# Optimization experiments

Hardware: AMD Instinct MI355X
Metric: run time of the kernel (lower is better)

Reference implementation:

```python
import jax, jax.numpy as jnp
import numpy as np

FANOUT = 10
NT = [61952, 5632, 512]      # targets produced by layer i
NN = [681472, 61952, 5632]   # input nodes consumed by layer i
NE = [619520, 56320, 5120]   # sampled edges for layer i (NT[i]*FANOUT)
IN_DIM = 256
HID = 256
NCLS = 47
EPS = 1e-5


def setup_inputs() -> dict:
    key = jax.random.key(0)
    ks = jax.random.split(key, 16)
    inp = {}
    inp['x_feat'] = jax.random.normal(ks[0], (NN[0], IN_DIM), jnp.float32)
    for i in range(3):
        # each target samples exactly FANOUT neighbors -> dst is repeat(arange)
        inp[f'src{i}'] = jax.random.randint(ks[1 + i], (NE[i],), 0, NN[i], dtype=jnp.int32)
        inp[f'dst{i}'] = jnp.repeat(jnp.arange(NT[i], dtype=jnp.int32), FANOUT)
        inp[f'tlid{i}'] = jax.random.randint(ks[4 + i], (NT[i],), 0, NN[i], dtype=jnp.int32)
        d_in = IN_DIM if i == 0 else HID
        s = 1.0 / np.sqrt(d_in)
        inp[f'Wl{i}'] = jax.random.uniform(ks[7 + i], (d_in, HID), jnp.float32, -s, s)
        inp[f'Wr{i}'] = jax.random.uniform(ks[10 + i], (d_in, HID), jnp.float32, -s, s)
        inp[f'b{i}'] = jnp.zeros((HID,), jnp.float32)
        inp[f'g{i}'] = jnp.ones((HID,), jnp.float32)
        inp[f'be{i}'] = jnp.zeros((HID,), jnp.float32)
    sf = 1.0 / np.sqrt(HID)
    inp['fc_w'] = jax.random.uniform(ks[13], (HID, NCLS), jnp.float32, -sf, sf)
    inp['fc_b'] = jnp.zeros((NCLS,), jnp.float32)
    return inp


def _sage_bn_relu(x, src, dst, tlid, Wl, Wr, b, g, be, n_t):
    # gather neighbor messages and mean-aggregate per target (SAGEConv, mean aggr)
    msg = x[src]                                               # [E, d_in]
    agg = jax.ops.segment_sum(msg, dst, num_segments=n_t)      # [T, d_in]
    cnt = jax.ops.segment_sum(jnp.ones(src.shape, x.dtype), dst, num_segments=n_t)
    agg = agg / jnp.maximum(cnt, 1.0)[:, None]
    x_tgt = x[tlid]                                            # F.embedding gather of target feats
    h = agg @ Wl + x_tgt @ Wr + b                              # lin_l(agg) + lin_r(x_target)
    # BatchNorm1d in training mode (biased batch stats)
    mu = h.mean(axis=0)
    var = h.var(axis=0)
    h = (h - mu) * jax.lax.rsqrt(var + EPS) * g + be
    return jax.nn.relu(h)


def reference(x_feat, src0, dst0, tlid0, src1, dst1, tlid1, src2, dst2, tlid2,
              Wl0, Wr0, b0, g0, be0, Wl1, Wr1, b1, g1, be1, Wl2, Wr2, b2, g2, be2,
              fc_w, fc_b):
    x = x_feat
    layers = [
        (src0, dst0, tlid0, Wl0, Wr0, b0, g0, be0, NT[0]),
        (src1, dst1, tlid1, Wl1, Wr1, b1, g1, be1, NT[1]),
        (src2, dst2, tlid2, Wl2, Wr2, b2, g2, be2, NT[2]),
    ]
    for (src, dst, tlid, Wl, Wr, b, g, be, n_t) in layers:
        x = _sage_bn_relu(x, src, dst, tlid, Wl, Wr, b, g, be, n_t)
    out = x @ fc_w + fc_b                                      # [B, class_count]
    return out
```

## Files before the change

### kernel.cpp

```cpp
#include <hip/hip_runtime.h>

#define HID 256
#define FANOUT 10

typedef __attribute__((ext_vector_type(8))) short bf16x8;
typedef __attribute__((ext_vector_type(4))) float f32x4;

__device__ __forceinline__ unsigned short f2bf(float f) {
    unsigned int u = __float_as_uint(f);
    u += 0x7FFFu + ((u >> 16) & 1u);
    return (unsigned short)(u >> 16);
}

__device__ __forceinline__ void gld_lds16(const void* g, void* l) {
    __builtin_amdgcn_global_load_lds((const __attribute__((address_space(1))) void*)g,
                                     (__attribute__((address_space(3))) void*)l, 16, 0, 0);
}

__global__ __launch_bounds__(256)
void agg_gather_kernel(const float* __restrict__ x, const int* __restrict__ src,
                       const int* __restrict__ tlid, unsigned short* __restrict__ Ag,
                       int T, const float* __restrict__ scal,
                       const float* __restrict__ shft, int apply) {
    const int wave = threadIdx.x >> 6, lane = threadIdx.x & 63;
    const int t = blockIdx.x * 4 + wave;
    if (t >= T) return;
    const float4* x4 = (const float4*)x;
    float4 sc = make_float4(1.f, 1.f, 1.f, 1.f);
    float4 sh = make_float4(0.f, 0.f, 0.f, 0.f);
    if (apply) {
        sc = ((const float4*)scal)[lane];
        sh = ((const float4*)shft)[lane];
    }
    const int* sp = src + (size_t)t * FANOUT;
    float sx = 0.f, sy = 0.f, sz = 0.f, sw = 0.f;
#pragma unroll
    for (int j = 0; j < FANOUT; ++j) {
        float4 v = x4[(size_t)sp[j] * 64 + lane];
        if (apply) {
            v.x = fmaxf(fmaf(v.x, sc.x, sh.x), 0.f);
            v.y = fmaxf(fmaf(v.y, sc.y, sh.y), 0.f);
            v.z = fmaxf(fmaf(v.z, sc.z, sh.z), 0.f);
            v.w = fmaxf(fmaf(v.w, sc.w, sh.w), 0.f);
        }
        sx += v.x; sy += v.y; sz += v.z; sw += v.w;
    }
    float4 tv = x4[(size_t)tlid[t] * 64 + lane];
    if (apply) {
        tv.x = fmaxf(fmaf(tv.x, sc.x, sh.x), 0.f);
        tv.y = fmaxf(fmaf(tv.y, sc.y, sh.y), 0.f);
        tv.z = fmaxf(fmaf(tv.z, sc.z, sh.z), 0.f);
        tv.w = fmaxf(fmaf(tv.w, sc.w, sh.w), 0.f);
    }

    const int rb = t >> 6;
    const int i  = (t & 63) >> 4;
    const int m0 = t & 15;
    const int cl   = lane >> 3;
    const int quad = (lane >> 1) & 3;
    const int j0   = (lane & 1) * 4;
    const int lf   = quad * 16 + m0;
    const size_t base = (size_t)rb * 32768 + (size_t)i * 512 + (size_t)lf * 8 + j0;

    ushort4 oa, ot;
    oa.x = f2bf(sx * 0.1f); oa.y = f2bf(sy * 0.1f);
    oa.z = f2bf(sz * 0.1f); oa.w = f2bf(sw * 0.1f);
    ot.x = f2bf(tv.x); ot.y = f2bf(tv.y); ot.z = f2bf(tv.z); ot.w = f2bf(tv.w);
    *(ushort4*)&Ag[base + (size_t)cl * 2048]       = oa;
    *(ushort4*)&Ag[base + (size_t)(cl + 8) * 2048] = ot;
}

__global__ __launch_bounds__(256)
void convw_all_kernel(const float* __restrict__ Wl0, const float* __restrict__ Wr0,
                      const float* __restrict__ Wl1, const float* __restrict__ Wr1,
                      const float* __restrict__ Wl2, const float* __restrict__ Wr2,
                      unsigned short* __restrict__ Wt) {
    const int idx = blockIdx.x * 256 + threadIdx.x;
    const int layer = idx >> 17, r = idx & 131071;
    const float* Wl = (layer == 0) ? Wl0 : (layer == 1) ? Wl1 : Wl2;
    const float* Wr = (layer == 0) ? Wr0 : (layer == 1) ? Wr1 : Wr2;
    const int kc = r & 31, n = (r >> 5) & 255, c = r >> 13;
    const int k = c * 32 + kc;
    const float v = (k < 256) ? Wl[k * 256 + n] : Wr[(k - 256) * 256 + n];
    Wt[idx] = f2bf(v);
}

__global__ __launch_bounds__(256)
void gemm_mfma_kernel(const unsigned short* __restrict__ Ag,
                      const unsigned short* __restrict__ Wt,
                      float* __restrict__ hbuf,
                      float* __restrict__ ssum, float* __restrict__ ssq) {
    __shared__ unsigned short Alds[2048];
    __shared__ unsigned short Blds[8192];
    const int tid = threadIdx.x, wave = tid >> 6, lane = tid & 63;
    const size_t rb = blockIdx.x;

    f32x4 acc[4][4];
#pragma unroll
    for (int a = 0; a < 4; ++a)
#pragma unroll
        for (int b = 0; b < 4; ++b) acc[a][b] = (f32x4){0.f, 0.f, 0.f, 0.f};

    const unsigned short* Abase = Ag + rb * 32768;
    const int soff = wave * 512 + lane * 8;

    for (int c = 0; c < 16; ++c) {
        __syncthreads();
        gld_lds16(Abase + (size_t)c * 2048 + soff, &Alds[wave * 512]);
        const unsigned short* Bb = Wt + (size_t)c * 8192;
#pragma unroll
        for (int ii = 0; ii < 4; ++ii)
            gld_lds16(Bb + ii * 2048 + soff, &Blds[ii * 2048 + wave * 512]);
        __syncthreads();

        bf16x8 af[4], bfr[4];
#pragma unroll
        for (int mi = 0; mi < 4; ++mi)
            af[mi] = *(const bf16x8*)&Alds[(mi * 64 + lane) * 8];
        const int nb = wave * 64 + (lane & 15);
        const int ko = (lane >> 4) * 8;
#pragma unroll
        for (int t = 0; t < 4; ++t)
            bfr[t] = *(const bf16x8*)&Blds[(nb + t * 16) * 32 + ko];

#pragma unroll
        for (int mi = 0; mi < 4; ++mi)
#pragma unroll
            for (int t = 0; t < 4; ++t)
                acc[mi][t] = __builtin_amdgcn_mfma_f32_16x16x32_bf16(
                    af[mi], bfr[t], acc[mi][t], 0, 0, 0);
    }

    const int q = lane >> 4, m0 = lane & 15;

#pragma unroll
    for (int t = 0; t < 4; ++t) {
        const int col = wave * 64 + t * 16 + m0;
#pragma unroll
        for (int mi = 0; mi < 4; ++mi) {
            float* op = hbuf + (rb * 64 + (size_t)mi * 16 + q * 4) * 256 + col;
#pragma unroll
            for (int r = 0; r < 4; ++r)
                op[(size_t)r * 256] = acc[mi][t][r];
        }
    }

    float s[4], sq[4];
#pragma unroll
    for (int t = 0; t < 4; ++t) {
        float a = 0.f, b = 0.f;
#pragma unroll
        for (int mi = 0; mi < 4; ++mi)
#pragma unroll
            for (int r = 0; r < 4; ++r) {
                const float v = acc[mi][t][r];
                a += v; b += v * v;
            }
        s[t] = a; sq[t] = b;
    }
#pragma unroll
    for (int t = 0; t < 4; ++t) {
        s[t] += __shfl_xor(s[t], 16);  s[t] += __shfl_xor(s[t], 32);
        sq[t] += __shfl_xor(sq[t], 16); sq[t] += __shfl_xor(sq[t], 32);
    }
    if (lane < 16) {
#pragma unroll
        for (int t = 0; t < 4; ++t) {
            const int col = wave * 64 + t * 16 + m0;
            atomicAdd(&ssum[col], s[t]);
            atomicAdd(&ssq[col], sq[t]);
        }
    }
}

__global__ void zero_kernel(float* p) { p[threadIdx.x] = 0.f; }

__global__ void bnfin_kernel(const float* __restrict__ ssum, const float* __restrict__ ssq,
                             const float* __restrict__ g, const float* __restrict__ be,
                             float* __restrict__ scal, float* __restrict__ shft,
                             float invT) {
    const int c = threadIdx.x;
    const float mu = ssum[c] * invT;
    float var = ssq[c] * invT - mu * mu;
    var = fmaxf(var, 0.f);
    const float rs = rsqrtf(var + 1e-5f);
    const float sc = rs * g[c];
    scal[c] = sc;
    shft[c] = be[c] - mu * sc;
}

__global__ __launch_bounds__(64)
void fc_kernel(const float* __restrict__ x, const float* __restrict__ scal,
               const float* __restrict__ shft, const float* __restrict__ w,
               const float* __restrict__ b, float* __restrict__ out, int C) {
    __shared__ float row[HID];
    const int r = blockIdx.x;
    const int tid = threadIdx.x;
    float4 v = ((const float4*)(x + (size_t)r * HID))[tid];
    const float4 sc = ((const float4*)scal)[tid];
    const float4 sh = ((const float4*)shft)[tid];
    v.x = fmaxf(fmaf(v.x, sc.x, sh.x), 0.f);
    v.y = fmaxf(fmaf(v.y, sc.y, sh.y), 0.f);
    v.z = fmaxf(fmaf(v.z, sc.z, sh.z), 0.f);
    v.w = fmaxf(fmaf(v.w, sc.w, sh.w), 0.f);
    ((float4*)row)[tid] = v;
    __syncthreads();
    if (tid < C) {
        float acc = b[tid];
#pragma unroll 8
        for (int k = 0; k < HID; ++k)
            acc = fmaf(row[k], w[k * C + tid], acc);
        out[(size_t)r * C + tid] = acc;
    }
}

extern "C" void kernel_launch(void* const* d_in, const int* in_sizes, int n_in,
                              void* d_out, int out_size, void* d_ws, size_t ws_size,
                              hipStream_t stream) {
    const float* x_feat = (const float*)d_in[0];
    const int T0 = in_sizes[3];
    const int T1 = in_sizes[11];
    const int T2 = in_sizes[19];
    const int NCLS = in_sizes[26];

    float* buf0 = (float*)d_ws;
    float* buf1 = buf0 + (size_t)T0 * HID;
    float* buf2 = buf1 + (size_t)T1 * HID;
    float* ssum = buf2 + (size_t)T2 * HID;
    float* ssq  = ssum + HID;
    float* scal = ssq + HID;
    float* shft = scal + HID;
    unsigned short* Wt = (unsigned short*)(shft + HID + 256);
    unsigned short* Ag = Wt + 3 * 512 * 256;

    const float* xs[3]   = { x_feat, buf0, buf1 };
    float*       bufs[3] = { buf0, buf1, buf2 };
    const int    Ts[3]   = { T0, T1, T2 };

    convw_all_kernel<<<1536, 256, 0, stream>>>(
        (const float*)d_in[4],  (const float*)d_in[5],
        (const float*)d_in[12], (const float*)d_in[13],
        (const float*)d_in[20], (const float*)d_in[21], Wt);

    for (int i = 0; i < 3; ++i) {
        const int base = 1 + i * 8;
        const int*   src  = (const int*)d_in[base + 0];
        const int*   tlid = (const int*)d_in[base + 2];
        const float* g    = (const float*)d_in[base + 6];
        const float* be   = (const float*)d_in[base + 7];
        const int T = Ts[i];

        agg_gather_kernel<<<(T + 3) / 4, 256, 0, stream>>>(
            xs[i], src, tlid, Ag, T, scal, shft, i > 0 ? 1 : 0);
        zero_kernel<<<1, 512, 0, stream>>>(ssum);
        gemm_mfma_kernel<<<T / 64, 256, 0, stream>>>(
            Ag, Wt + (size_t)i * 131072, bufs[i], ssum, ssq);
        bnfin_kernel<<<1, HID, 0, stream>>>(ssum, ssq, g, be, scal, shft, 1.0f / (float)T);
    }

    const float* fc_w = (const float*)d_in[25];
    const float* fc_b = (const float*)d_in[26];
    fc_kernel<<<T2, 64, 0, stream>>>(buf2, scal, shft, fc_w, fc_b, (float*)d_out, NCLS);
}
```

Baseline: 1.063 ms.

## Fuse neighbor gather-aggregation into GEMM kernel via shared-memory A tile

Merges the gather/mean-aggregate kernel into the MFMA GEMM kernel. Each block builds its full 64x512 bf16 A tile in LDS (64 KB) from the gathered features, then runs the GEMM reading B fragments directly from global memory instead of staging them through LDS. This removes the global write and read of the intermediate Ag buffer and one launch per layer. In exchange, each wave gathers its 16 targets serially, so there is less memory-level parallelism per block, and the large LDS footprint lowers occupancy.

After: 1.027 ms. 1.04x faster.

```diff
diff --git a/kernel.cpp b/kernel.cpp
--- a/kernel.cpp
+++ b/kernel.cpp
@@ -10,64 +10,6 @@
     unsigned int u = __float_as_uint(f);
     u += 0x7FFFu + ((u >> 16) & 1u);
     return (unsigned short)(u >> 16);
-}
-
-__device__ __forceinline__ void gld_lds16(const void* g, void* l) {
-    __builtin_amdgcn_global_load_lds((const __attribute__((address_space(1))) void*)g,
-                                     (__attribute__((address_space(3))) void*)l, 16, 0, 0);
-}
-
-__global__ __launch_bounds__(256)
-void agg_gather_kernel(const float* __restrict__ x, const int* __restrict__ src,
-                       const int* __restrict__ tlid, unsigned short* __restrict__ Ag,
-                       int T, const float* __restrict__ scal,
-                       const float* __restrict__ shft, int apply) {
-    const int wave = threadIdx.x >> 6, lane = threadIdx.x & 63;
-    const int t = blockIdx.x * 4 + wave;
-    if (t >= T) return;
-    const float4* x4 = (const float4*)x;
-    float4 sc = make_float4(1.f, 1.f, 1.f, 1.f);
-    float4 sh = make_float4(0.f, 0.f, 0.f, 0.f);
-    if (apply) {
-        sc = ((const float4*)scal)[lane];
-        sh = ((const float4*)shft)[lane];
-    }
-    const int* sp = src + (size_t)t * FANOUT;
-    float sx = 0.f, sy = 0.f, sz = 0.f, sw = 0.f;
-#pragma unroll
-    for (int j = 0; j < FANOUT; ++j) {
-        float4 v = x4[(size_t)sp[j] * 64 + lane];
-        if (apply) {
-            v.x = fmaxf(fmaf(v.x, sc.x, sh.x), 0.f);
-            v.y = fmaxf(fmaf(v.y, sc.y, sh.y), 0.f);
-            v.z = fmaxf(fmaf(v.z, sc.z, sh.z), 0.f);
-            v.w = fmaxf(fmaf(v.w, sc.w, sh.w), 0.f);
-        }
-        sx += v.x; sy += v.y; sz += v.z; sw += v.w;
-    }
-    float4 tv = x4[(size_t)tlid[t] * 64 + lane];
-    if (apply) {
-        tv.x = fmaxf(fmaf(tv.x, sc.x, sh.x), 0.f);
-        tv.y = fmaxf(fmaf(tv.y, sc.y, sh.y), 0.f);
-        tv.z = fmaxf(fmaf(tv.z, sc.z, sh.z), 0.f);
-        tv.w = fmaxf(fmaf(tv.w, sc.w, sh.w), 0.f);
-    }
-
-    const int rb = t >> 6;
-    const int i  = (t & 63) >> 4;
-    const int m0 = t & 15;
-    const int cl   = lane >> 3;
-    const int quad = (lane >> 1) & 3;
-    const int j0   = (lane & 1) * 4;
-    const int lf   = quad * 16 + m0;
-    const size_t base = (size_t)rb * 32768 + (size_t)i * 512 + (size_t)lf * 8 + j0;
-
-    ushort4 oa, ot;
-    oa.x = f2bf(sx * 0.1f); oa.y = f2bf(sy * 0.1f);
-    oa.z = f2bf(sz * 0.1f); oa.w = f2bf(sw * 0.1f);
-    ot.x = f2bf(tv.x); ot.y = f2bf(tv.y); ot.z = f2bf(tv.z); ot.w = f2bf(tv.w);
-    *(ushort4*)&Ag[base + (size_t)cl * 2048]       = oa;
-    *(ushort4*)&Ag[base + (size_t)(cl + 8) * 2048] = ot;
 }
 
 __global__ __launch_bounds__(256)
@@ -86,43 +28,77 @@
 }
 
 __global__ __launch_bounds__(256)
-void gemm_mfma_kernel(const unsigned short* __restrict__ Ag,
-                      const unsigned short* __restrict__ Wt,
-                      float* __restrict__ hbuf,
-                      float* __restrict__ ssum, float* __restrict__ ssq) {
-    __shared__ unsigned short Alds[2048];
-    __shared__ unsigned short Blds[8192];
+void fused_layer_kernel(const float* __restrict__ x, const int* __restrict__ src,
+                        const int* __restrict__ tlid,
+                        const unsigned short* __restrict__ Wt,
+                        float* __restrict__ hbuf,
+                        float* __restrict__ ssum, float* __restrict__ ssq,
+                        const float* __restrict__ scal,
+                        const float* __restrict__ shft, int apply) {
+    __shared__ unsigned short Alds[32768];
     const int tid = threadIdx.x, wave = tid >> 6, lane = tid & 63;
     const size_t rb = blockIdx.x;
 
+    const float4* x4 = (const float4*)x;
+    float4 sc = make_float4(1.f, 1.f, 1.f, 1.f);
+    float4 sh = make_float4(0.f, 0.f, 0.f, 0.f);
+    if (apply) {
+        sc = ((const float4*)scal)[lane];
+        sh = ((const float4*)shft)[lane];
+    }
+    const int cl = lane >> 3;
+    const int quad = (lane >> 1) & 3;
+    const int j0 = (lane & 1) * 4;
+
+    for (int ti = 0; ti < 16; ++ti) {
+        const int t = (int)rb * 64 + wave * 16 + ti;
+        const int* sp = src + (size_t)t * FANOUT;
+        float sx = 0.f, sy = 0.f, sz = 0.f, sw = 0.f;
+#pragma unroll
+        for (int j = 0; j < FANOUT; ++j) {
+            float4 v = x4[(size_t)sp[j] * 64 + lane];
+            if (apply) {
+                v.x = fmaxf(fmaf(v.x, sc.x, sh.x), 0.f);
+                v.y = fmaxf(fmaf(v.y, sc.y, sh.y), 0.f);
+                v.z = fmaxf(fmaf(v.z, sc.z, sh.z), 0.f);
+                v.w = fmaxf(fmaf(v.w, sc.w, sh.w), 0.f);
+            }
+            sx += v.x; sy += v.y; sz += v.z; sw += v.w;
+        }
+        float4 tv = x4[(size_t)tlid[t] * 64 + lane];
+        if (apply) {
+            tv.x = fmaxf(fmaf(tv.x, sc.x, sh.x), 0.f);
+            tv.y = fmaxf(fmaf(tv.y, sc.y, sh.y), 0.f);
+            tv.z = fmaxf(fmaf(tv.z, sc.z, sh.z), 0.f);
+            tv.w = fmaxf(fmaf(tv.w, sc.w, sh.w), 0.f);
+        }
+        ushort4 oa, ot;
+        oa.x = f2bf(sx * 0.1f); oa.y = f2bf(sy * 0.1f);
+        oa.z = f2bf(sz * 0.1f); oa.w = f2bf(sw * 0.1f);
+        ot.x = f2bf(tv.x); ot.y = f2bf(tv.y); ot.z = f2bf(tv.z); ot.w = f2bf(tv.w);
+        const int base = wave * 512 + (quad * 16 + ti) * 8 + j0;
+        *(ushort4*)&Alds[cl * 2048 + base]       = oa;
+        *(ushort4*)&Alds[(cl + 8) * 2048 + base] = ot;
+    }
+    __syncthreads();
+
     f32x4 acc[4][4];
 #pragma unroll
     for (int a = 0; a < 4; ++a)
 #pragma unroll
         for (int b = 0; b < 4; ++b) acc[a][b] = (f32x4){0.f, 0.f, 0.f, 0.f};
 
-    const unsigned short* Abase = Ag + rb * 32768;
-    const int soff = wave * 512 + lane * 8;
-
+    const int nb = wave * 64 + (lane & 15);
+    const int ko = (lane >> 4) * 8;
+#pragma unroll
     for (int c = 0; c < 16; ++c) {
-        __syncthreads();
-        gld_lds16(Abase + (size_t)c * 2048 + soff, &Alds[wave * 512]);
-        const unsigned short* Bb = Wt + (size_t)c * 8192;
-#pragma unroll
-        for (int ii = 0; ii < 4; ++ii)
-            gld_lds16(Bb + ii * 2048 + soff, &Blds[ii * 2048 + wave * 512]);
-        __syncthreads();
-
         bf16x8 af[4], bfr[4];
 #pragma unroll
         for (int mi = 0; mi < 4; ++mi)
-            af[mi] = *(const bf16x8*)&Alds[(mi * 64 + lane) * 8];
-        const int nb = wave * 64 + (lane & 15);
-        const int ko = (lane >> 4) * 8;
+            af[mi] = *(const bf16x8*)&Alds[c * 2048 + mi * 512 + lane * 8];
 #pragma unroll
         for (int t = 0; t < 4; ++t)
-            bfr[t] = *(const bf16x8*)&Blds[(nb + t * 16) * 32 + ko];
-
+            bfr[t] = *(const bf16x8*)&Wt[(size_t)c * 8192 + (nb + t * 16) * 32 + ko];
 #pragma unroll
         for (int mi = 0; mi < 4; ++mi)
 #pragma unroll
@@ -132,7 +108,6 @@
     }
 
     const int q = lane >> 4, m0 = lane & 15;
-
 #pragma unroll
     for (int t = 0; t < 4; ++t) {
         const int col = wave * 64 + t * 16 + m0;
@@ -231,7 +206,6 @@
     float* scal = ssq + HID;
     float* shft = scal + HID;
     unsigned short* Wt = (unsigned short*)(shft + HID + 256);
-    unsigned short* Ag = Wt + 3 * 512 * 256;
 
     const float* xs[3]   = { x_feat, buf0, buf1 };
     float*       bufs[3] = { buf0, buf1, buf2 };
@@ -250,11 +224,10 @@
         const float* be   = (const float*)d_in[base + 7];
         const int T = Ts[i];
 
-        agg_gather_kernel<<<(T + 3) / 4, 256, 0, stream>>>(
-            xs[i], src, tlid, Ag, T, scal, shft, i > 0 ? 1 : 0);
         zero_kernel<<<1, 512, 0, stream>>>(ssum);
-        gemm_mfma_kernel<<<T / 64, 256, 0, stream>>>(
-            Ag, Wt + (size_t)i * 131072, bufs[i], ssum, ssq);
+        fused_layer_kernel<<<T / 64, 256, 0, stream>>>(
+            xs[i], src, tlid, Wt + (size_t)i * 131072, bufs[i],
+            ssum, ssq, scal, shft, i > 0 ? 1 : 0);
         bnfin_kernel<<<1, HID, 0, stream>>>(ssum, ssq, g, be, scal, shft, 1.0f / (float)T);
     }
 
```
